# Optimization experiments

Hardware: AMD Instinct MI355X
Metric: run time of the kernel (lower is better)

Reference implementation:

```python
import jax, jax.numpy as jnp
import numpy as np

N = 100_000   # nodes
E = 600_000   # edges
F_IN = 128
H_ENC = 256
D = 128       # embedding dim
R_HOPS = 3
N_CLS = 40

def setup_inputs() -> dict:
    key = jax.random.key(0)
    ks = jax.random.split(key, 12)
    def lin(k, fi, fo):  # kaiming-ish init
        return jax.random.normal(k, (fi, fo), dtype=jnp.float32) * (1.0 / np.sqrt(fi))
    x = jax.random.normal(ks[0], (N, F_IN), dtype=jnp.float32)
    edge_index = jax.random.randint(ks[1], (2, E), 0, N, dtype=jnp.int32)
    enc_w1 = lin(ks[2], F_IN, H_ENC); enc_b1 = jnp.zeros((H_ENC,), jnp.float32)
    enc_w2 = lin(ks[3], H_ENC, D);    enc_b2 = jnp.zeros((D,), jnp.float32)
    gcn_w = jnp.stack([lin(ks[4 + r], D, D) for r in range(R_HOPS)])  # [R, D, D]
    gcn_b = jnp.zeros((R_HOPS, D), jnp.float32)
    dec_w1 = lin(ks[8], D, D);        dec_b1 = jnp.zeros((D,), jnp.float32)
    dec_w2 = lin(ks[9], D, N_CLS);    dec_b2 = jnp.zeros((N_CLS,), jnp.float32)
    return {"x": x, "edge_index": edge_index,
            "enc_w1": enc_w1, "enc_b1": enc_b1, "enc_w2": enc_w2, "enc_b2": enc_b2,
            "gcn_w": gcn_w, "gcn_b": gcn_b,
            "dec_w1": dec_w1, "dec_b1": dec_b1, "dec_w2": dec_w2, "dec_b2": dec_b2}

def reference(x, edge_index, enc_w1, enc_b1, enc_w2, enc_b2,
              gcn_w, gcn_b, dec_w1, dec_b1, dec_w2, dec_b2):
    src, dst = edge_index[0], edge_index[1]
    # encoder MLP (norm=None): Linear -> ReLU -> Linear
    h = jax.nn.relu(x @ enc_w1 + enc_b1)
    h = h @ enc_w2 + enc_b2
    # r-hop GCNConv (normalize=False): transform -> gather(src) -> scatter_add(dst) -> +bias, then ReLU
    for r in range(R_HOPS):
        hw = h @ gcn_w[r]                                   # [N, D]
        msg = hw[src]                                       # [E, D] gather
        agg = jax.ops.segment_sum(msg, dst, num_segments=N)  # [N, D] scatter-add
        h = jax.nn.relu(agg + gcn_b[r])                     # dropout p=0 / eval -> identity
    # decoder MLP: Linear -> ReLU -> Linear
    h = jax.nn.relu(h @ dec_w1 + dec_b1)
    logits = h @ dec_w2 + dec_b2                            # [N, 40]
    return jax.nn.log_softmax(logits, axis=1)
```

## Files before the change

### kernel.cpp

```cpp
#include <hip/hip_runtime.h>
#include <hip/hip_bf16.h>
#include <cstddef>

typedef __attribute__((ext_vector_type(8))) short short8v;
typedef __attribute__((ext_vector_type(4))) float f32x4;

__device__ inline ushort f2bf(float f) {
    uint u = __float_as_uint(f);
    uint r = (u + 0x7fffu + ((u >> 16) & 1u)) >> 16;
    return (ushort)r;
}
__device__ inline float bflo(uint v) { return __uint_as_float(v << 16); }
__device__ inline float bfhi(uint v) { return __uint_as_float(v & 0xffff0000u); }

__global__ __launch_bounds__(256) void cast_bf16_kernel(
    const float* __restrict__ in, ushort* __restrict__ out, int n4)
{
    int i = blockIdx.x * 256 + threadIdx.x;
    if (i >= n4) return;
    float4 v = ((const float4*)in)[i];
    ushort4 o = { f2bf(v.x), f2bf(v.y), f2bf(v.z), f2bf(v.w) };
    ((ushort4*)out)[i] = o;
}

__global__ __launch_bounds__(256) void wtrans_kernel(
    const float* __restrict__ W, ushort* __restrict__ Wt,
    int K, int Nout, int rows)
{
    int idx = blockIdx.x * 256 + threadIdx.x;
    if (idx >= rows * K) return;
    int r = idx / K;
    int c = idx - r * K;
    float v = (r < Nout) ? W[(size_t)c * Nout + r] : 0.f;
    Wt[idx] = f2bf(v);
}

template <bool RELU, int NT, int KT, bool OUTF32, bool BIAS>
__global__ __launch_bounds__(512) void dense_mfma5_kernel(
    const ushort* __restrict__ A, const ushort* __restrict__ Wt,
    const float* __restrict__ bias, void* __restrict__ Cout,
    int M, int Ncols)
{
    constexpr int KSTEPS = KT / 32;
    constexpr int ROWS_B = NT * 16;
    constexpr int ROW_BYTES = KT * 2;
    constexpr int CHUNKS_PER_ROW = ROW_BYTES / 16;

    __shared__ __align__(16) char lds[ROWS_B * ROW_BYTES];

    const int tid  = threadIdx.x;
    const int lane = tid & 63;
    const int wave = tid >> 6;
    const int fr   = lane & 15;
    const int fq   = lane >> 4;
    const int cb   = blockIdx.y * ROWS_B;

    {
        constexpr int TOTAL = ROWS_B * CHUNKS_PER_ROW;
        #pragma unroll
        for (int c0 = 0; c0 < TOTAL; c0 += 512) {
            int c = c0 + tid;
            if (TOTAL % 512 != 0 && c >= TOTAL) break;
            int r = c / CHUNKS_PER_ROW;
            int w = c - r * CHUNKS_PER_ROW;
            short8v v = *(const short8v*)(Wt + (size_t)(cb + r) * KT + w * 8);
            int dstByte = r * ROW_BYTES + ((w * 16) ^ ((r & 7) << 4));
            *(short8v*)(lds + dstByte) = v;
        }
    }
    __syncthreads();

    const int rowblk = blockIdx.x * 128 + wave * 16;

    short8v aReg[KSTEPS];
    {
        int r = rowblk + fr;
        if (r >= M) r = M - 1;
        #pragma unroll
        for (int ks = 0; ks < KSTEPS; ++ks)
            aReg[ks] = *(const short8v*)(A + (size_t)r * KT + ks * 32 + fq * 8);
    }

    f32x4 acc[NT];
    #pragma unroll
    for (int n = 0; n < NT; ++n) acc[n] = (f32x4){0.f, 0.f, 0.f, 0.f};

    #pragma unroll
    for (int ks = 0; ks < KSTEPS; ++ks) {
        const int kByte = ks * 64 + fq * 16;
        short8v b[NT];
        #pragma unroll
        for (int n = 0; n < NT; ++n) {
            int lr = n * 16 + fr;
            b[n] = *(const short8v*)(lds + lr * ROW_BYTES + (kByte ^ ((lr & 7) << 4)));
        }
        #pragma unroll
        for (int n = 0; n < NT; ++n)
            acc[n] = __builtin_amdgcn_mfma_f32_16x16x32_bf16(aReg[ks], b[n], acc[n], 0, 0, 0);
    }

    float bv[NT];
    #pragma unroll
    for (int n = 0; n < NT; ++n) {
        int col = cb + n * 16 + fr;
        bv[n] = (BIAS && col < Ncols) ? bias[col] : 0.f;
    }

    if constexpr (!OUTF32) {
        __syncthreads();
        constexpr int SROW = NT * 32;
        char* scratch = lds + wave * (16 * SROW);
        #pragma unroll
        for (int n = 0; n < NT; ++n) {
            #pragma unroll
            for (int j = 0; j < 4; ++j) {
                int row = fq * 4 + j;
                float v = acc[n][j] + bv[n];
                if (RELU) v = fmaxf(v, 0.f);
                int byte = (n * 32 + fr * 2) ^ ((row & 3) << 5);
                *(ushort*)(scratch + row * SROW + byte) = f2bf(v);
            }
        }
        constexpr int LPR = 2 * NT;
        constexpr int RPI = 64 / LPR;
        constexpr int NI  = 16 / RPI;
        #pragma unroll
        for (int i2 = 0; i2 < NI; ++i2) {
            int row = i2 * RPI + lane / LPR;
            int k16 = lane % LPR;
            int rb  = row * SROW + ((k16 * 16) ^ ((row & 3) << 5));
            short8v vv = *(const short8v*)(scratch + rb);
            int gr = rowblk + row;
            if (gr < M)
                *(short8v*)((char*)Cout + (size_t)gr * (Ncols * 2) + cb * 2 + k16 * 16) = vv;
        }
    } else {
        const int rbase = rowblk + fq * 4;
        #pragma unroll
        for (int n = 0; n < NT; ++n) {
            int col = cb + n * 16 + fr;
            #pragma unroll
            for (int j = 0; j < 4; ++j) {
                int r = rbase + j;
                float v = acc[n][j] + bv[n];
                if (RELU) v = fmaxf(v, 0.f);
                if (r < M && col < Ncols)
                    ((float*)Cout)[(size_t)r * Ncols + col] = v;
            }
        }
    }
}

__global__ __launch_bounds__(256) void degree_kernel(
    const int* __restrict__ dst, int* __restrict__ cnt, int E)
{
    int e = blockIdx.x * 256 + threadIdx.x;
    if (e < E) atomicAdd(&cnt[dst[e]], 1);
}

__global__ __launch_bounds__(256) void scan_block_kernel(
    const int* __restrict__ cnt, int* __restrict__ rs,
    int* __restrict__ partials, int N)
{
    __shared__ int sm[256];
    int i = blockIdx.x * 256 + threadIdx.x;
    int v = (i < N) ? cnt[i] : 0;
    sm[threadIdx.x] = v;
    __syncthreads();
    #pragma unroll
    for (int off = 1; off < 256; off <<= 1) {
        int t = (threadIdx.x >= off) ? sm[threadIdx.x - off] : 0;
        __syncthreads();
        sm[threadIdx.x] += t;
        __syncthreads();
    }
    if (i < N) rs[i] = sm[threadIdx.x] - v;
    if (threadIdx.x == 255) partials[blockIdx.x] = sm[255];
}

__global__ __launch_bounds__(512) void scan_partials_kernel(
    int* __restrict__ partials, int nblk)
{
    __shared__ int sm[512];
    int v = (threadIdx.x < nblk) ? partials[threadIdx.x] : 0;
    sm[threadIdx.x] = v;
    __syncthreads();
    #pragma unroll
    for (int off = 1; off < 512; off <<= 1) {
        int t = (threadIdx.x >= off) ? sm[threadIdx.x - off] : 0;
        __syncthreads();
        sm[threadIdx.x] += t;
        __syncthreads();
    }
    if (threadIdx.x < nblk) partials[threadIdx.x] = sm[threadIdx.x] - v;
}

__global__ __launch_bounds__(256) void add_offsets_kernel(
    int* __restrict__ rs, const int* __restrict__ partials, int N, int E)
{
    int i = blockIdx.x * 256 + threadIdx.x;
    if (i < N) rs[i] += partials[blockIdx.x];
    if (i == N) rs[N] = E;
}

__global__ __launch_bounds__(256) void fill_kernel(
    const int* __restrict__ src, const int* __restrict__ dst,
    const int* __restrict__ rs, int* __restrict__ cursor,
    int* __restrict__ csr_src, int E)
{
    int e = blockIdx.x * 256 + threadIdx.x;
    if (e >= E) return;
    int d = dst[e];
    int pos = rs[d] + atomicAdd(&cursor[d], 1);
    csr_src[pos] = src[e];
}

__global__ __launch_bounds__(256) void gather_agg2_kernel(
    const ushort* __restrict__ hw, const int* __restrict__ csr_src,
    const int* __restrict__ rs, const float* __restrict__ bias,
    ushort* __restrict__ hout, int N)
{
    int wid  = (blockIdx.x * 256 + threadIdx.x) >> 6;
    int lane = threadIdx.x & 63;
    int node = wid * 2 + (lane >> 5);
    if (node >= N) return;
    int sl = lane & 31;
    int beg = rs[node];
    int end = rs[node + 1];

    float a0 = 0.f, a1 = 0.f, a2 = 0.f, a3 = 0.f;
    int i = beg;
    for (; i + 4 <= end; i += 4) {
        int s0 = csr_src[i + 0];
        int s1 = csr_src[i + 1];
        int s2 = csr_src[i + 2];
        int s3 = csr_src[i + 3];
        uint2 v0 = *(const uint2*)(hw + (size_t)s0 * 128 + sl * 4);
        uint2 v1 = *(const uint2*)(hw + (size_t)s1 * 128 + sl * 4);
        uint2 v2 = *(const uint2*)(hw + (size_t)s2 * 128 + sl * 4);
        uint2 v3 = *(const uint2*)(hw + (size_t)s3 * 128 + sl * 4);
        a0 += bflo(v0.x) + bflo(v1.x) + bflo(v2.x) + bflo(v3.x);
        a1 += bfhi(v0.x) + bfhi(v1.x) + bfhi(v2.x) + bfhi(v3.x);
        a2 += bflo(v0.y) + bflo(v1.y) + bflo(v2.y) + bflo(v3.y);
        a3 += bfhi(v0.y) + bfhi(v1.y) + bfhi(v2.y) + bfhi(v3.y);
    }
    if (i + 2 <= end) {
        int s0 = csr_src[i + 0];
        int s1 = csr_src[i + 1];
        uint2 v0 = *(const uint2*)(hw + (size_t)s0 * 128 + sl * 4);
        uint2 v1 = *(const uint2*)(hw + (size_t)s1 * 128 + sl * 4);
        a0 += bflo(v0.x) + bflo(v1.x);
        a1 += bfhi(v0.x) + bfhi(v1.x);
        a2 += bflo(v0.y) + bflo(v1.y);
        a3 += bfhi(v0.y) + bfhi(v1.y);
        i += 2;
    }
    if (i < end) {
        int s0 = csr_src[i];
        uint2 v0 = *(const uint2*)(hw + (size_t)s0 * 128 + sl * 4);
        a0 += bflo(v0.x);
        a1 += bfhi(v0.x);
        a2 += bflo(v0.y);
        a3 += bfhi(v0.y);
    }

    float4 bb = ((const float4*)bias)[sl];
    a0 = fmaxf(a0 + bb.x, 0.f);
    a1 = fmaxf(a1 + bb.y, 0.f);
    a2 = fmaxf(a2 + bb.z, 0.f);
    a3 = fmaxf(a3 + bb.w, 0.f);
    uint2 o;
    o.x = (uint)f2bf(a0) | ((uint)f2bf(a1) << 16);
    o.y = (uint)f2bf(a2) | ((uint)f2bf(a3) << 16);
    *(uint2*)(hout + (size_t)node * 128 + sl * 4) = o;
}

__global__ __launch_bounds__(256) void log_softmax_kernel(
    const float* __restrict__ logits, float* __restrict__ out, int M)
{
    int w    = (int)(((long long)blockIdx.x * 256 + threadIdx.x) >> 6);
    int lane = threadIdx.x & 63;
    if (w >= M) return;
    float v = -3.402823466e38f;
    if (lane < 40) v = logits[(size_t)w * 40 + lane];
    float m = v;
    #pragma unroll
    for (int off = 32; off > 0; off >>= 1) m = fmaxf(m, __shfl_xor(m, off, 64));
    float e = (lane < 40) ? expf(v - m) : 0.f;
    float s = e;
    #pragma unroll
    for (int off = 32; off > 0; off >>= 1) s += __shfl_xor(s, off, 64);
    float ls = logf(s);
    if (lane < 40) out[(size_t)w * 40 + lane] = v - m - ls;
}

extern "C" void kernel_launch(void* const* d_in, const int* in_sizes, int n_in,
                              void* d_out, int out_size, void* d_ws, size_t ws_size,
                              hipStream_t stream)
{
    const float* x      = (const float*)d_in[0];
    const int*   edge   = (const int*)d_in[1];
    const float* enc_w1 = (const float*)d_in[2];
    const float* enc_b1 = (const float*)d_in[3];
    const float* enc_w2 = (const float*)d_in[4];
    const float* enc_b2 = (const float*)d_in[5];
    const float* gcn_w  = (const float*)d_in[6];
    const float* gcn_b  = (const float*)d_in[7];
    const float* dec_w1 = (const float*)d_in[8];
    const float* dec_b1 = (const float*)d_in[9];
    const float* dec_w2 = (const float*)d_in[10];
    const float* dec_b2 = (const float*)d_in[11];

    const int F_IN = 128, H_ENC = 256, D = 128, N_CLS = 40, R = 3;
    const int N = in_sizes[0] / F_IN;
    const int E = in_sizes[1] / 2;
    const int* src = edge;
    const int* dst = edge + E;

    char* p = (char*)d_ws;
    ushort* xb     = (ushort*)p;                 p += (size_t)N * 128 * 2;
    ushort* h1     = (ushort*)p;                 p += (size_t)N * 256 * 2;
    ushort* h      = (ushort*)p;                 p += (size_t)N * 128 * 2;
    ushort* hw     = (ushort*)p;                 p += (size_t)N * 128 * 2;
    float*  logits = (float*)p;                  p += (size_t)N * 40 * 4;
    ushort* enc1t  = (ushort*)p;                 p += 256 * 128 * 2;
    ushort* enc2t  = (ushort*)p;                 p += 128 * 256 * 2;
    ushort* gcnt   = (ushort*)p;                 p += 3 * 128 * 128 * 2;
    ushort* dec1t  = (ushort*)p;                 p += 128 * 128 * 2;
    ushort* dec2t  = (ushort*)p;                 p += 48 * 128 * 2;
    int* csr_src   = (int*)p;
    int* rs        = csr_src + E;
    int* cnt       = rs + (N + 1);
    int* partials  = cnt + N;

    float* out = (float*)d_out;
    dim3 blk(256);
    dim3 blk512(512);

    cast_bf16_kernel<<<(N * 128 / 4 + 255) / 256, blk, 0, stream>>>(x, xb, N * 128 / 4);
    wtrans_kernel<<<(256 * 128 + 255) / 256, blk, 0, stream>>>(enc_w1, enc1t, 128, 256, 256);
    wtrans_kernel<<<(128 * 256 + 255) / 256, blk, 0, stream>>>(enc_w2, enc2t, 256, 128, 128);
    for (int r = 0; r < R; ++r)
        wtrans_kernel<<<(128 * 128 + 255) / 256, blk, 0, stream>>>(
            gcn_w + (size_t)r * 128 * 128, gcnt + (size_t)r * 128 * 128, 128, 128, 128);
    wtrans_kernel<<<(128 * 128 + 255) / 256, blk, 0, stream>>>(dec_w1, dec1t, 128, 128, 128);
    wtrans_kernel<<<(48 * 128 + 255) / 256, blk, 0, stream>>>(dec_w2, dec2t, 128, 40, 48);

    const int nblkN = (N + 255) / 256;
    const int nblkE = (E + 255) / 256;
    hipMemsetAsync(cnt, 0, (size_t)N * sizeof(int), stream);
    degree_kernel<<<nblkE, blk, 0, stream>>>(dst, cnt, E);
    scan_block_kernel<<<nblkN, blk, 0, stream>>>(cnt, rs, partials, N);
    scan_partials_kernel<<<1, 512, 0, stream>>>(partials, nblkN);
    add_offsets_kernel<<<nblkN + 1, blk, 0, stream>>>(rs, partials, N, E);
    hipMemsetAsync(cnt, 0, (size_t)N * sizeof(int), stream);
    fill_kernel<<<nblkE, blk, 0, stream>>>(src, dst, rs, cnt, csr_src, E);

    const int gdx = (N + 127) / 128;

    dense_mfma5_kernel<true, 8, 128, false, true><<<dim3(gdx, 2), blk512, 0, stream>>>(
        xb, enc1t, enc_b1, h1, N, 256);
    dense_mfma5_kernel<false, 4, 256, false, true><<<dim3(gdx, 2), blk512, 0, stream>>>(
        h1, enc2t, enc_b2, h, N, 128);

    const int aggb = ((N + 1) / 2 * 64 + 255) / 256;
    for (int r = 0; r < R; ++r) {
        dense_mfma5_kernel<false, 8, 128, false, false><<<dim3(gdx, 1), blk512, 0, stream>>>(
            h, gcnt + (size_t)r * 128 * 128, nullptr, hw, N, 128);
        gather_agg2_kernel<<<aggb, blk, 0, stream>>>(
            hw, csr_src, rs, gcn_b + (size_t)r * 128, h, N);
    }

    dense_mfma5_kernel<true, 8, 128, false, true><<<dim3(gdx, 1), blk512, 0, stream>>>(
        h, dec1t, dec_b1, hw , N, 128);
    dense_mfma5_kernel<false, 3, 128, true, true><<<dim3(gdx, 1), blk512, 0, stream>>>(
        hw, dec2t, dec_b2, logits, N, 40);

    const int smb = (N + 3) / 4;
    log_softmax_kernel<<<smb, blk, 0, stream>>>(logits, out, N);
}
```

Before: 414.3 us.

## Fuse GCN aggregate-then-transform hops, softmax into decoder, and prep kernels

Each GCN hop now aggregates neighbour rows first and then applies the weight matmul in one kernel, using linearity (A·(hW) = (A·h)W), so the separate hw buffer round-trip and one launch per hop go away. The fp32→bf16 cast of x is folded into the first encoder GEMM, log-softmax is fused into the final decoder GEMM, all weight transposes run as one launch, and the CSR offset scan/cursor init is merged so one memset is dropped. The cost is that the aggregation now runs in a thread layout tied to the MFMA operand (16 nodes per wave, 4 lanes per node), which may give poorer gather parallelism and more load imbalance across high-degree nodes. The neighbour sum is also rounded to bf16 before the matmul, which changes rounding slightly.

```diff
diff --git a/kernel.cpp b/kernel.cpp
--- a/kernel.cpp
+++ b/kernel.cpp
@@ -13,32 +13,34 @@
 __device__ inline float bflo(uint v) { return __uint_as_float(v << 16); }
 __device__ inline float bfhi(uint v) { return __uint_as_float(v & 0xffff0000u); }
 
-__global__ __launch_bounds__(256) void cast_bf16_kernel(
-    const float* __restrict__ in, ushort* __restrict__ out, int n4)
-{
-    int i = blockIdx.x * 256 + threadIdx.x;
-    if (i >= n4) return;
-    float4 v = ((const float4*)in)[i];
-    ushort4 o = { f2bf(v.x), f2bf(v.y), f2bf(v.z), f2bf(v.w) };
-    ((ushort4*)out)[i] = o;
-}
-
-__global__ __launch_bounds__(256) void wtrans_kernel(
-    const float* __restrict__ W, ushort* __restrict__ Wt,
-    int K, int Nout, int rows)
-{
+__global__ __launch_bounds__(256) void wtrans_all_kernel(
+    const float* __restrict__ w1, const float* __restrict__ w2,
+    const float* __restrict__ gw, const float* __restrict__ d1,
+    const float* __restrict__ d2, ushort* __restrict__ arena)
+{
+    const int y = blockIdx.y;
+    const float* W; int K, Nout, rows; size_t dst;
+    switch (y) {
+        case 0: W = w1; K = 128; Nout = 256; rows = 256; dst = 0;      break;
+        case 1: W = w2; K = 256; Nout = 128; rows = 128; dst = 32768;  break;
+        case 2: case 3: case 4:
+            W = gw + (size_t)(y - 2) * 16384; K = 128; Nout = 128; rows = 128;
+            dst = 65536 + (size_t)(y - 2) * 16384;                     break;
+        case 5: W = d1; K = 128; Nout = 128; rows = 128; dst = 114688; break;
+        default: W = d2; K = 128; Nout = 40; rows = 48; dst = 131072;  break;
+    }
     int idx = blockIdx.x * 256 + threadIdx.x;
     if (idx >= rows * K) return;
     int r = idx / K;
     int c = idx - r * K;
     float v = (r < Nout) ? W[(size_t)c * Nout + r] : 0.f;
-    Wt[idx] = f2bf(v);
-}
-
-template <bool RELU, int NT, int KT, bool OUTF32, bool BIAS>
+    arena[dst + idx] = f2bf(v);
+}
+
+template <bool RELU, int NT, int KT, bool AF32, bool BIAS>
 __global__ __launch_bounds__(512) void dense_mfma5_kernel(
-    const ushort* __restrict__ A, const ushort* __restrict__ Wt,
-    const float* __restrict__ bias, void* __restrict__ Cout,
+    const void* __restrict__ A, const ushort* __restrict__ Wt,
+    const float* __restrict__ bias, ushort* __restrict__ Cout,
     int M, int Ncols)
 {
     constexpr int KSTEPS = KT / 32;
@@ -76,9 +78,25 @@
     {
         int r = rowblk + fr;
         if (r >= M) r = M - 1;
-        #pragma unroll
-        for (int ks = 0; ks < KSTEPS; ++ks)
-            aReg[ks] = *(const short8v*)(A + (size_t)r * KT + ks * 32 + fq * 8);
+        if constexpr (AF32) {
+            const float* Af = (const float*)A;
+            #pragma unroll
+            for (int ks = 0; ks < KSTEPS; ++ks) {
+                float4 p0 = *(const float4*)(Af + (size_t)r * KT + ks * 32 + fq * 8);
+                float4 p1 = *(const float4*)(Af + (size_t)r * KT + ks * 32 + fq * 8 + 4);
+                short8v o;
+                o[0] = (short)f2bf(p0.x); o[1] = (short)f2bf(p0.y);
+                o[2] = (short)f2bf(p0.z); o[3] = (short)f2bf(p0.w);
+                o[4] = (short)f2bf(p1.x); o[5] = (short)f2bf(p1.y);
+                o[6] = (short)f2bf(p1.z); o[7] = (short)f2bf(p1.w);
+                aReg[ks] = o;
+            }
+        } else {
+            const ushort* Ab = (const ushort*)A;
+            #pragma unroll
+            for (int ks = 0; ks < KSTEPS; ++ks)
+                aReg[ks] = *(const short8v*)(Ab + (size_t)r * KT + ks * 32 + fq * 8);
+        }
     }
 
     f32x4 acc[NT];
@@ -106,47 +124,248 @@
         bv[n] = (BIAS && col < Ncols) ? bias[col] : 0.f;
     }
 
-    if constexpr (!OUTF32) {
-        __syncthreads();
-        constexpr int SROW = NT * 32;
-        char* scratch = lds + wave * (16 * SROW);
+    __syncthreads();
+    constexpr int SROW = NT * 32;
+    char* scratch = lds + wave * (16 * SROW);
+    #pragma unroll
+    for (int n = 0; n < NT; ++n) {
+        #pragma unroll
+        for (int j = 0; j < 4; ++j) {
+            int row = fq * 4 + j;
+            float v = acc[n][j] + bv[n];
+            if (RELU) v = fmaxf(v, 0.f);
+            int byte = (n * 32 + fr * 2) ^ ((row & 3) << 5);
+            *(ushort*)(scratch + row * SROW + byte) = f2bf(v);
+        }
+    }
+    constexpr int LPR = 2 * NT;
+    constexpr int RPI = 64 / LPR;
+    constexpr int NI  = 16 / RPI;
+    #pragma unroll
+    for (int i2 = 0; i2 < NI; ++i2) {
+        int row = i2 * RPI + lane / LPR;
+        int k16 = lane % LPR;
+        int rb  = row * SROW + ((k16 * 16) ^ ((row & 3) << 5));
+        short8v vv = *(const short8v*)(scratch + rb);
+        int gr = rowblk + row;
+        if (gr < M)
+            *(short8v*)((char*)Cout + (size_t)gr * (Ncols * 2) + cb * 2 + k16 * 16) = vv;
+    }
+}
+
+__global__ __launch_bounds__(512, 4) void gcn_hop_kernel(
+    const ushort* __restrict__ h, const ushort* __restrict__ Wt,
+    const int* __restrict__ csr_src, const int* __restrict__ rs,
+    const float* __restrict__ bias, ushort* __restrict__ hout, int N)
+{
+    constexpr int NT = 8, KT = 128, KSTEPS = 4;
+    constexpr int ROWS_B = 128, ROW_BYTES = 256, CHUNKS_PER_ROW = 16;
+
+    __shared__ __align__(16) char lds[ROWS_B * ROW_BYTES];
+
+    const int tid  = threadIdx.x;
+    const int lane = tid & 63;
+    const int wave = tid >> 6;
+    const int fr   = lane & 15;
+    const int fq   = lane >> 4;
+
+    {
+        constexpr int TOTAL = ROWS_B * CHUNKS_PER_ROW;
+        #pragma unroll
+        for (int c0 = 0; c0 < TOTAL; c0 += 512) {
+            int c = c0 + tid;
+            int r = c / CHUNKS_PER_ROW;
+            int w = c - r * CHUNKS_PER_ROW;
+            short8v v = *(const short8v*)(Wt + (size_t)r * KT + w * 8);
+            int dstByte = r * ROW_BYTES + ((w * 16) ^ ((r & 7) << 4));
+            *(short8v*)(lds + dstByte) = v;
+        }
+    }
+
+    const int rowblk = blockIdx.x * 128 + wave * 16;
+    const int node   = rowblk + fr;
+    int beg = 0, end = 0;
+    if (node < N) { beg = rs[node]; end = rs[node + 1]; }
+
+    float sf[KSTEPS][8];
+    #pragma unroll
+    for (int ks = 0; ks < KSTEPS; ++ks)
+        #pragma unroll
+        for (int e = 0; e < 8; ++e) sf[ks][e] = 0.f;
+
+    int i = beg;
+    for (; i + 2 <= end; i += 2) {
+        int s0 = csr_src[i + 0];
+        int s1 = csr_src[i + 1];
+        const ushort* h0 = h + (size_t)s0 * 128;
+        const ushort* h1 = h + (size_t)s1 * 128;
+        #pragma unroll
+        for (int ks = 0; ks < KSTEPS; ++ks) {
+            uint4 q0 = *(const uint4*)(h0 + ks * 32 + fq * 8);
+            uint4 q1 = *(const uint4*)(h1 + ks * 32 + fq * 8);
+            sf[ks][0] += bflo(q0.x) + bflo(q1.x);
+            sf[ks][1] += bfhi(q0.x) + bfhi(q1.x);
+            sf[ks][2] += bflo(q0.y) + bflo(q1.y);
+            sf[ks][3] += bfhi(q0.y) + bfhi(q1.y);
+            sf[ks][4] += bflo(q0.z) + bflo(q1.z);
+            sf[ks][5] += bfhi(q0.z) + bfhi(q1.z);
+            sf[ks][6] += bflo(q0.w) + bflo(q1.w);
+            sf[ks][7] += bfhi(q0.w) + bfhi(q1.w);
+        }
+    }
+    if (i < end) {
+        int s0 = csr_src[i];
+        const ushort* h0 = h + (size_t)s0 * 128;
+        #pragma unroll
+        for (int ks = 0; ks < KSTEPS; ++ks) {
+            uint4 q0 = *(const uint4*)(h0 + ks * 32 + fq * 8);
+            sf[ks][0] += bflo(q0.x); sf[ks][1] += bfhi(q0.x);
+            sf[ks][2] += bflo(q0.y); sf[ks][3] += bfhi(q0.y);
+            sf[ks][4] += bflo(q0.z); sf[ks][5] += bfhi(q0.z);
+            sf[ks][6] += bflo(q0.w); sf[ks][7] += bfhi(q0.w);
+        }
+    }
+
+    short8v aReg[KSTEPS];
+    #pragma unroll
+    for (int ks = 0; ks < KSTEPS; ++ks) {
+        short8v o;
+        #pragma unroll
+        for (int e = 0; e < 8; ++e) o[e] = (short)f2bf(sf[ks][e]);
+        aReg[ks] = o;
+    }
+
+    f32x4 acc[NT];
+    #pragma unroll
+    for (int n = 0; n < NT; ++n) acc[n] = (f32x4){0.f, 0.f, 0.f, 0.f};
+
+    __syncthreads();
+
+    #pragma unroll
+    for (int ks = 0; ks < KSTEPS; ++ks) {
+        const int kByte = ks * 64 + fq * 16;
+        short8v b[NT];
         #pragma unroll
         for (int n = 0; n < NT; ++n) {
-            #pragma unroll
-            for (int j = 0; j < 4; ++j) {
-                int row = fq * 4 + j;
-                float v = acc[n][j] + bv[n];
-                if (RELU) v = fmaxf(v, 0.f);
-                int byte = (n * 32 + fr * 2) ^ ((row & 3) << 5);
-                *(ushort*)(scratch + row * SROW + byte) = f2bf(v);
-            }
-        }
-        constexpr int LPR = 2 * NT;
-        constexpr int RPI = 64 / LPR;
-        constexpr int NI  = 16 / RPI;
-        #pragma unroll
-        for (int i2 = 0; i2 < NI; ++i2) {
-            int row = i2 * RPI + lane / LPR;
-            int k16 = lane % LPR;
-            int rb  = row * SROW + ((k16 * 16) ^ ((row & 3) << 5));
-            short8v vv = *(const short8v*)(scratch + rb);
-            int gr = rowblk + row;
-            if (gr < M)
-                *(short8v*)((char*)Cout + (size_t)gr * (Ncols * 2) + cb * 2 + k16 * 16) = vv;
-        }
-    } else {
-        const int rbase = rowblk + fq * 4;
+            int lr = n * 16 + fr;
+            b[n] = *(const short8v*)(lds + lr * ROW_BYTES + (kByte ^ ((lr & 7) << 4)));
+        }
+        #pragma unroll
+        for (int n = 0; n < NT; ++n)
+            acc[n] = __builtin_amdgcn_mfma_f32_16x16x32_bf16(aReg[ks], b[n], acc[n], 0, 0, 0);
+    }
+
+    float bv[NT];
+    #pragma unroll
+    for (int n = 0; n < NT; ++n) bv[n] = bias[n * 16 + fr];
+
+    __syncthreads();
+    constexpr int SROW = NT * 32;
+    char* scratch = lds + wave * (16 * SROW);
+    #pragma unroll
+    for (int n = 0; n < NT; ++n) {
+        #pragma unroll
+        for (int j = 0; j < 4; ++j) {
+            int row = fq * 4 + j;
+            float v = fmaxf(acc[n][j] + bv[n], 0.f);
+            int byte = (n * 32 + fr * 2) ^ ((row & 3) << 5);
+            *(ushort*)(scratch + row * SROW + byte) = f2bf(v);
+        }
+    }
+    constexpr int LPR = 16, RPI = 4, NI = 4;
+    #pragma unroll
+    for (int i2 = 0; i2 < NI; ++i2) {
+        int row = i2 * RPI + lane / LPR;
+        int k16 = lane % LPR;
+        int rb  = row * SROW + ((k16 * 16) ^ ((row & 3) << 5));
+        short8v vv = *(const short8v*)(scratch + rb);
+        int gr = rowblk + row;
+        if (gr < N)
+            *(short8v*)((char*)hout + (size_t)gr * 256 + k16 * 16) = vv;
+    }
+}
+
+__global__ __launch_bounds__(512) void dense_dec2sm_kernel(
+    const ushort* __restrict__ A, const ushort* __restrict__ Wt,
+    const float* __restrict__ bias, float* __restrict__ out, int M)
+{
+    constexpr int NT = 3, KT = 128, KSTEPS = 4;
+    constexpr int ROWS_B = 48, ROW_BYTES = 256, CHUNKS_PER_ROW = 16;
+
+    __shared__ __align__(16) char lds[ROWS_B * ROW_BYTES];
+
+    const int tid  = threadIdx.x;
+    const int lane = tid & 63;
+    const int wave = tid >> 6;
+    const int fr   = lane & 15;
+    const int fq   = lane >> 4;
+
+    {
+        constexpr int TOTAL = ROWS_B * CHUNKS_PER_ROW;
+        #pragma unroll
+        for (int c0 = 0; c0 < TOTAL; c0 += 512) {
+            int c = c0 + tid;
+            if (c >= TOTAL) break;
+            int r = c / CHUNKS_PER_ROW;
+            int w = c - r * CHUNKS_PER_ROW;
+            short8v v = *(const short8v*)(Wt + (size_t)r * KT + w * 8);
+            int dstByte = r * ROW_BYTES + ((w * 16) ^ ((r & 7) << 4));
+            *(short8v*)(lds + dstByte) = v;
+        }
+    }
+    __syncthreads();
+
+    const int rowblk = blockIdx.x * 128 + wave * 16;
+
+    short8v aReg[KSTEPS];
+    {
+        int r = rowblk + fr;
+        if (r >= M) r = M - 1;
+        #pragma unroll
+        for (int ks = 0; ks < KSTEPS; ++ks)
+            aReg[ks] = *(const short8v*)(A + (size_t)r * KT + ks * 32 + fq * 8);
+    }
+
+    f32x4 acc[NT];
+    #pragma unroll
+    for (int n = 0; n < NT; ++n) acc[n] = (f32x4){0.f, 0.f, 0.f, 0.f};
+
+    #pragma unroll
+    for (int ks = 0; ks < KSTEPS; ++ks) {
+        const int kByte = ks * 64 + fq * 16;
+        short8v b[NT];
         #pragma unroll
         for (int n = 0; n < NT; ++n) {
-            int col = cb + n * 16 + fr;
-            #pragma unroll
-            for (int j = 0; j < 4; ++j) {
-                int r = rbase + j;
-                float v = acc[n][j] + bv[n];
-                if (RELU) v = fmaxf(v, 0.f);
-                if (r < M && col < Ncols)
-                    ((float*)Cout)[(size_t)r * Ncols + col] = v;
-            }
+            int lr = n * 16 + fr;
+            b[n] = *(const short8v*)(lds + lr * ROW_BYTES + (kByte ^ ((lr & 7) << 4)));
+        }
+        #pragma unroll
+        for (int n = 0; n < NT; ++n)
+            acc[n] = __builtin_amdgcn_mfma_f32_16x16x32_bf16(aReg[ks], b[n], acc[n], 0, 0, 0);
+    }
+
+    float bv0 = bias[fr];
+    float bv1 = bias[16 + fr];
+    float bv2 = (fr < 8) ? bias[32 + fr] : 0.f;
+    const float NEG = -3.402823466e38f;
+
+    #pragma unroll
+    for (int j = 0; j < 4; ++j) {
+        int row = rowblk + fq * 4 + j;
+        float v0 = acc[0][j] + bv0;
+        float v1 = acc[1][j] + bv1;
+        float v2 = (fr < 8) ? (acc[2][j] + bv2) : NEG;
+        float m = fmaxf(fmaxf(v0, v1), v2);
+        #pragma unroll
+        for (int off = 1; off < 16; off <<= 1) m = fmaxf(m, __shfl_xor(m, off, 64));
+        float s = expf(v0 - m) + expf(v1 - m) + ((fr < 8) ? expf(v2 - m) : 0.f);
+        #pragma unroll
+        for (int off = 1; off < 16; off <<= 1) s += __shfl_xor(s, off, 64);
+        float ls = m + logf(s);
+        if (row < M) {
+            out[(size_t)row * 40 + fr]      = v0 - ls;
+            out[(size_t)row * 40 + 16 + fr] = v1 - ls;
+            if (fr < 8) out[(size_t)row * 40 + 32 + fr] = v2 - ls;
         }
     }
 }
@@ -178,8 +397,9 @@
     if (threadIdx.x == 255) partials[blockIdx.x] = sm[255];
 }
 
-__global__ __launch_bounds__(512) void scan_partials_kernel(
-    int* __restrict__ partials, int nblk)
+__global__ __launch_bounds__(512) void add_offsets2_kernel(
+    int* __restrict__ rs, const int* __restrict__ partials,
+    int* __restrict__ cursor, int N, int E, int nblk)
 {
     __shared__ int sm[512];
     int v = (threadIdx.x < nblk) ? partials[threadIdx.x] : 0;
@@ -192,106 +412,28 @@
         sm[threadIdx.x] += t;
         __syncthreads();
     }
-    if (threadIdx.x < nblk) partials[threadIdx.x] = sm[threadIdx.x] - v;
-}
-
-__global__ __launch_bounds__(256) void add_offsets_kernel(
-    int* __restrict__ rs, const int* __restrict__ partials, int N, int E)
-{
-    int i = blockIdx.x * 256 + threadIdx.x;
-    if (i < N) rs[i] += partials[blockIdx.x];
+    int excl = sm[threadIdx.x] - v;
+    __syncthreads();
+    sm[threadIdx.x] = excl;
+    __syncthreads();
+    int i = blockIdx.x * 512 + threadIdx.x;
+    if (i < N) {
+        int r2 = rs[i] + sm[i >> 8];
+        rs[i] = r2;
+        cursor[i] = r2;
+    }
     if (i == N) rs[N] = E;
 }
 
 __global__ __launch_bounds__(256) void fill_kernel(
     const int* __restrict__ src, const int* __restrict__ dst,
-    const int* __restrict__ rs, int* __restrict__ cursor,
-    int* __restrict__ csr_src, int E)
+    int* __restrict__ cursor, int* __restrict__ csr_src, int E)
 {
     int e = blockIdx.x * 256 + threadIdx.x;
     if (e >= E) return;
     int d = dst[e];
-    int pos = rs[d] + atomicAdd(&cursor[d], 1);
+    int pos = atomicAdd(&cursor[d], 1);
     csr_src[pos] = src[e];
-}
-
-__global__ __launch_bounds__(256) void gather_agg2_kernel(
-    const ushort* __restrict__ hw, const int* __restrict__ csr_src,
-    const int* __restrict__ rs, const float* __restrict__ bias,
-    ushort* __restrict__ hout, int N)
-{
-    int wid  = (blockIdx.x * 256 + threadIdx.x) >> 6;
-    int lane = threadIdx.x & 63;
-    int node = wid * 2 + (lane >> 5);
-    if (node >= N) return;
-    int sl = lane & 31;
-    int beg = rs[node];
-    int end = rs[node + 1];
-
-    float a0 = 0.f, a1 = 0.f, a2 = 0.f, a3 = 0.f;
-    int i = beg;
-    for (; i + 4 <= end; i += 4) {
-        int s0 = csr_src[i + 0];
-        int s1 = csr_src[i + 1];
-        int s2 = csr_src[i + 2];
-        int s3 = csr_src[i + 3];
-        uint2 v0 = *(const uint2*)(hw + (size_t)s0 * 128 + sl * 4);
-        uint2 v1 = *(const uint2*)(hw + (size_t)s1 * 128 + sl * 4);
-        uint2 v2 = *(const uint2*)(hw + (size_t)s2 * 128 + sl * 4);
-        uint2 v3 = *(const uint2*)(hw + (size_t)s3 * 128 + sl * 4);
-        a0 += bflo(v0.x) + bflo(v1.x) + bflo(v2.x) + bflo(v3.x);
-        a1 += bfhi(v0.x) + bfhi(v1.x) + bfhi(v2.x) + bfhi(v3.x);
-        a2 += bflo(v0.y) + bflo(v1.y) + bflo(v2.y) + bflo(v3.y);
-        a3 += bfhi(v0.y) + bfhi(v1.y) + bfhi(v2.y) + bfhi(v3.y);
-    }
-    if (i + 2 <= end) {
-        int s0 = csr_src[i + 0];
-        int s1 = csr_src[i + 1];
-        uint2 v0 = *(const uint2*)(hw + (size_t)s0 * 128 + sl * 4);
-        uint2 v1 = *(const uint2*)(hw + (size_t)s1 * 128 + sl * 4);
-        a0 += bflo(v0.x) + bflo(v1.x);
-        a1 += bfhi(v0.x) + bfhi(v1.x);
-        a2 += bflo(v0.y) + bflo(v1.y);
-        a3 += bfhi(v0.y) + bfhi(v1.y);
-        i += 2;
-    }
-    if (i < end) {
-        int s0 = csr_src[i];
-        uint2 v0 = *(const uint2*)(hw + (size_t)s0 * 128 + sl * 4);
-        a0 += bflo(v0.x);
-        a1 += bfhi(v0.x);
-        a2 += bflo(v0.y);
-        a3 += bfhi(v0.y);
-    }
-
-    float4 bb = ((const float4*)bias)[sl];
-    a0 = fmaxf(a0 + bb.x, 0.f);
-    a1 = fmaxf(a1 + bb.y, 0.f);
-    a2 = fmaxf(a2 + bb.z, 0.f);
-    a3 = fmaxf(a3 + bb.w, 0.f);
-    uint2 o;
-    o.x = (uint)f2bf(a0) | ((uint)f2bf(a1) << 16);
-    o.y = (uint)f2bf(a2) | ((uint)f2bf(a3) << 16);
-    *(uint2*)(hout + (size_t)node * 128 + sl * 4) = o;
-}
-
-__global__ __launch_bounds__(256) void log_softmax_kernel(
-    const float* __restrict__ logits, float* __restrict__ out, int M)
-{
-    int w    = (int)(((long long)blockIdx.x * 256 + threadIdx.x) >> 6);
-    int lane = threadIdx.x & 63;
-    if (w >= M) return;
-    float v = -3.402823466e38f;
-    if (lane < 40) v = logits[(size_t)w * 40 + lane];
-    float m = v;
-    #pragma unroll
-    for (int off = 32; off > 0; off >>= 1) m = fmaxf(m, __shfl_xor(m, off, 64));
-    float e = (lane < 40) ? expf(v - m) : 0.f;
-    float s = e;
-    #pragma unroll
-    for (int off = 32; off > 0; off >>= 1) s += __shfl_xor(s, off, 64);
-    float ls = logf(s);
-    if (lane < 40) out[(size_t)w * 40 + lane] = v - m - ls;
 }
 
 extern "C" void kernel_launch(void* const* d_in, const int* in_sizes, int n_in,
@@ -311,71 +453,61 @@
     const float* dec_w2 = (const float*)d_in[10];
     const float* dec_b2 = (const float*)d_in[11];
 
-    const int F_IN = 128, H_ENC = 256, D = 128, N_CLS = 40, R = 3;
+    const int F_IN = 128, R = 3;
     const int N = in_sizes[0] / F_IN;
     const int E = in_sizes[1] / 2;
     const int* src = edge;
     const int* dst = edge + E;
 
     char* p = (char*)d_ws;
-    ushort* xb     = (ushort*)p;                 p += (size_t)N * 128 * 2;
-    ushort* h1     = (ushort*)p;                 p += (size_t)N * 256 * 2;
-    ushort* h      = (ushort*)p;                 p += (size_t)N * 128 * 2;
-    ushort* hw     = (ushort*)p;                 p += (size_t)N * 128 * 2;
-    float*  logits = (float*)p;                  p += (size_t)N * 40 * 4;
-    ushort* enc1t  = (ushort*)p;                 p += 256 * 128 * 2;
-    ushort* enc2t  = (ushort*)p;                 p += 128 * 256 * 2;
-    ushort* gcnt   = (ushort*)p;                 p += 3 * 128 * 128 * 2;
-    ushort* dec1t  = (ushort*)p;                 p += 128 * 128 * 2;
-    ushort* dec2t  = (ushort*)p;                 p += 48 * 128 * 2;
-    int* csr_src   = (int*)p;
-    int* rs        = csr_src + E;
-    int* cnt       = rs + (N + 1);
-    int* partials  = cnt + N;
+    ushort* h1    = (ushort*)p;                  p += (size_t)N * 256 * 2;
+    ushort* hA    = (ushort*)p;                  p += (size_t)N * 128 * 2;
+    ushort* hB    = (ushort*)p;                  p += (size_t)N * 128 * 2;
+    ushort* arena = (ushort*)p;                  p += 137216 * 2;
+    int* csr_src  = (int*)p;                     p += (size_t)E * 4;
+    int* rs       = (int*)p;                     p += (size_t)(N + 1) * 4;
+    int* cnt      = (int*)p;                     p += (size_t)N * 4;
+    int* partials = (int*)p;
+
+    const ushort* enc1t = arena;
+    const ushort* enc2t = arena + 32768;
+    const ushort* gcnt  = arena + 65536;
+    const ushort* dec1t = arena + 114688;
+    const ushort* dec2t = arena + 131072;
 
     float* out = (float*)d_out;
     dim3 blk(256);
     dim3 blk512(512);
 
-    cast_bf16_kernel<<<(N * 128 / 4 + 255) / 256, blk, 0, stream>>>(x, xb, N * 128 / 4);
-    wtrans_kernel<<<(256 * 128 + 255) / 256, blk, 0, stream>>>(enc_w1, enc1t, 128, 256, 256);
-    wtrans_kernel<<<(128 * 256 + 255) / 256, blk, 0, stream>>>(enc_w2, enc2t, 256, 128, 128);
-    for (int r = 0; r < R; ++r)
-        wtrans_kernel<<<(128 * 128 + 255) / 256, blk, 0, stream>>>(
-            gcn_w + (size_t)r * 128 * 128, gcnt + (size_t)r * 128 * 128, 128, 128, 128);
-    wtrans_kernel<<<(128 * 128 + 255) / 256, blk, 0, stream>>>(dec_w1, dec1t, 128, 128, 128);
-    wtrans_kernel<<<(48 * 128 + 255) / 256, blk, 0, stream>>>(dec_w2, dec2t, 128, 40, 48);
+    wtrans_all_kernel<<<dim3(128, 7), blk, 0, stream>>>(
+        enc_w1, enc_w2, gcn_w, dec_w1, dec_w2, arena);
 
     const int nblkN = (N + 255) / 256;
     const int nblkE = (E + 255) / 256;
     hipMemsetAsync(cnt, 0, (size_t)N * sizeof(int), stream);
     degree_kernel<<<nblkE, blk, 0, stream>>>(dst, cnt, E);
     scan_block_kernel<<<nblkN, blk, 0, stream>>>(cnt, rs, partials, N);
-    scan_partials_kernel<<<1, 512, 0, stream>>>(partials, nblkN);
-    add_offsets_kernel<<<nblkN + 1, blk, 0, stream>>>(rs, partials, N, E);
-    hipMemsetAsync(cnt, 0, (size_t)N * sizeof(int), stream);
-    fill_kernel<<<nblkE, blk, 0, stream>>>(src, dst, rs, cnt, csr_src, E);
+    add_offsets2_kernel<<<(N + 1 + 511) / 512, blk512, 0, stream>>>(
+        rs, partials, cnt, N, E, nblkN);
+    fill_kernel<<<nblkE, blk, 0, stream>>>(src, dst, cnt, csr_src, E);
 
     const int gdx = (N + 127) / 128;
 
-    dense_mfma5_kernel<true, 8, 128, false, true><<<dim3(gdx, 2), blk512, 0, stream>>>(
-        xb, enc1t, enc_b1, h1, N, 256);
+    dense_mfma5_kernel<true, 8, 128, true, true><<<dim3(gdx, 2), blk512, 0, stream>>>(
+        x, enc1t, enc_b1, h1, N, 256);
     dense_mfma5_kernel<false, 4, 256, false, true><<<dim3(gdx, 2), blk512, 0, stream>>>(
-        h1, enc2t, enc_b2, h, N, 128);
-
-    const int aggb = ((N + 1) / 2 * 64 + 255) / 256;
+        h1, enc2t, enc_b2, hA, N, 128);
+
+    ushort* cur = hA;
+    ushort* nxt = hB;
     for (int r = 0; r < R; ++r) {
-        dense_mfma5_kernel<false, 8, 128, false, false><<<dim3(gdx, 1), blk512, 0, stream>>>(
-            h, gcnt + (size_t)r * 128 * 128, nullptr, hw, N, 128);
-        gather_agg2_kernel<<<aggb, blk, 0, stream>>>(
-            hw, csr_src, rs, gcn_b + (size_t)r * 128, h, N);
+        gcn_hop_kernel<<<gdx, blk512, 0, stream>>>(
+            cur, gcnt + (size_t)r * 16384, csr_src, rs, gcn_b + (size_t)r * 128, nxt, N);
+        ushort* t = cur; cur = nxt; nxt = t;
     }
 
     dense_mfma5_kernel<true, 8, 128, false, true><<<dim3(gdx, 1), blk512, 0, stream>>>(
-        h, dec1t, dec_b1, hw , N, 128);
-    dense_mfma5_kernel<false, 3, 128, true, true><<<dim3(gdx, 1), blk512, 0, stream>>>(
-        hw, dec2t, dec_b2, logits, N, 40);
-
-    const int smb = (N + 3) / 4;
-    log_softmax_kernel<<<smb, blk, 0, stream>>>(logits, out, N);
-}
+        cur, dec1t, dec_b1, nxt, N, 128);
+    dense_dec2sm_kernel<<<gdx, blk512, 0, stream>>>(
+        nxt, dec2t, dec_b2, out, N);
+}
```

Result: faster. 365.6 us (-11.8%).
